# Optimization experiments

Measured on AMD Instinct MI355X. Metric: run time of the kernel, lower is better.

The kernel has to match this reference:

```python
import jax, jax.numpy as jnp
import numpy as np
from jax import lax

LAMBDA = 1.0
N_ITER = 100
N, PDIM, QDIM = 4096, 128, 128


def setup_inputs() -> dict:
    key = jax.random.key(0)
    k1, k2, k3, k4, k5, k6 = jax.random.split(key, 6)
    return {
        "U": jax.random.normal(k1, (N, PDIM), dtype=jnp.float32),
        "V": jax.random.normal(k2, (N, QDIM), dtype=jnp.float32),
        "W": jax.random.uniform(k3, (N, N), dtype=jnp.float32),
        "mu": jax.random.uniform(k4, (N, 1), dtype=jnp.float32),
        "nu": jax.random.uniform(k5, (N, 1), dtype=jnp.float32),
        "A": jax.random.normal(k6, (PDIM, QDIM), dtype=jnp.float32),
    }


def reference(U, V, W, mu, nu, A):
    # Cost matrix: C = softplus(W - U A V^T)  -> (n, n)
    UV = jnp.einsum('np,pq,mq->nm', U, A, V)
    C = jax.nn.softplus(W - UV)
    K = jnp.exp(-LAMBDA * C)

    def step(carry, _):
        a, b = carry
        a = mu / (K @ b)          # (n,1)
        b = nu / (K.T @ a)        # (n,1)
        return (a, b), None

    init = (jnp.ones_like(mu), jnp.ones_like(nu))
    (a, b), _ = lax.scan(step, init, None, length=N_ITER)

    # plan = diag(a) @ K @ diag(b)  ==  a * K * b^T (outer-product scaling)
    plan = a * K * b.T
    return plan
```

## Files before the change

kernel.cpp:

```cpp
#include <hip/hip_runtime.h>
#include <hip/hip_bf16.h>
#include <stdint.h>

#define NDIM 4096
#define PD   128
#define TS   64
#define LDP  (PD + 4)

__device__ __forceinline__ float bf2f(unsigned int u16) {
    union { unsigned int i; float f; } v; v.i = u16 << 16; return v.f;
}
__device__ __forceinline__ unsigned short f2bf(float f) {
    union { float f; unsigned int i; } v; v.f = f;
    unsigned int x = v.i;
    return (unsigned short)((x + 0x7fffu + ((x >> 16) & 1u)) >> 16);
}

__global__ __launch_bounds__(128) void ua_kernel(
    const float* __restrict__ U, const float* __restrict__ A, float* __restrict__ UA)
{
    __shared__ float us[PD];
    const int i = blockIdx.x;
    const int q = threadIdx.x;
    us[q] = U[i * PD + q];
    __syncthreads();
    float acc = 0.f;
    #pragma unroll 8
    for (int p = 0; p < PD; ++p) acc += us[p] * A[p * PD + q];
    UA[i * PD + q] = acc;
}

__global__ __launch_bounds__(256) void buildK_kernel(
    const float* __restrict__ UA, const float* __restrict__ V,
    const float* __restrict__ W, unsigned short* __restrict__ K,
    unsigned short* __restrict__ KT)
{
    __shared__ float UAs[TS][LDP];
    __shared__ float Vs[TS][LDP];
    __shared__ float tileT[TS][TS + 1];
    const int i0 = blockIdx.y * TS, j0 = blockIdx.x * TS;
    const int t = threadIdx.x;

    for (int idx = t; idx < TS * PD / 4; idx += 256) {
        const int r = idx >> 5;
        const int c = (idx & 31) << 2;
        *(float4*)&UAs[r][c] = *(const float4*)&UA[(size_t)(i0 + r) * PD + c];
        *(float4*)&Vs[r][c]  = *(const float4*)&V[(size_t)(j0 + r) * PD + c];
    }
    __syncthreads();

    const int tx = t & 15, ty = t >> 4;
    float acc[4][4] = {};
    for (int p = 0; p < PD; p += 4) {
        float4 a4[4], b4[4];
        #pragma unroll
        for (int ii = 0; ii < 4; ++ii) a4[ii] = *(const float4*)&UAs[ty + 16 * ii][p];
        #pragma unroll
        for (int jj = 0; jj < 4; ++jj) b4[jj] = *(const float4*)&Vs[tx + 16 * jj][p];
        #pragma unroll
        for (int ii = 0; ii < 4; ++ii)
            #pragma unroll
            for (int jj = 0; jj < 4; ++jj)
                acc[ii][jj] += a4[ii].x * b4[jj].x + a4[ii].y * b4[jj].y
                             + a4[ii].z * b4[jj].z + a4[ii].w * b4[jj].w;
    }

    #pragma unroll
    for (int ii = 0; ii < 4; ++ii) {
        const int i = ty + 16 * ii;
        #pragma unroll
        for (int jj = 0; jj < 4; ++jj) {
            const int j = tx + 16 * jj;
            const float w = W[(size_t)(i0 + i) * NDIM + (j0 + j)];
            const float k = 1.0f / (1.0f + __expf(w - acc[ii][jj]));
            K[(size_t)(i0 + i) * NDIM + (j0 + j)] = f2bf(k);
            tileT[j][i] = k;
        }
    }
    __syncthreads();
    for (int idx = t; idx < TS * TS; idx += 256) {
        const int j = idx >> 6, i = idx & 63;
        KT[(size_t)(j0 + j) * NDIM + (i0 + i)] = f2bf(tileT[j][i]);
    }
}

__global__ __launch_bounds__(256) void init_ones_kernel(float* __restrict__ v) {
    v[blockIdx.x * 256 + threadIdx.x] = 1.0f;
}

__global__ __launch_bounds__(256) void matvec_div_kernel(
    const unsigned short* __restrict__ M, const float* __restrict__ vin,
    const float* __restrict__ num, float* __restrict__ vout)
{
    const int wave = threadIdx.x >> 6;
    const int lane = threadIdx.x & 63;
    const int row  = blockIdx.x * 4 + wave;
    const unsigned short* mrow = M + (size_t)row * NDIM;
    float acc = 0.f;
    #pragma unroll
    for (int pass = 0; pass < NDIM / (64 * 8); ++pass) {
        const int j0 = (pass * 64 + lane) * 8;
        const uint4  kv = *(const uint4*)&mrow[j0];
        const float4 b0 = *(const float4*)&vin[j0];
        const float4 b1 = *(const float4*)&vin[j0 + 4];
        acc += bf2f(kv.x & 0xffffu) * b0.x;
        acc += bf2f(kv.x >> 16)     * b0.y;
        acc += bf2f(kv.y & 0xffffu) * b0.z;
        acc += bf2f(kv.y >> 16)     * b0.w;
        acc += bf2f(kv.z & 0xffffu) * b1.x;
        acc += bf2f(kv.z >> 16)     * b1.y;
        acc += bf2f(kv.w & 0xffffu) * b1.z;
        acc += bf2f(kv.w >> 16)     * b1.w;
    }
    #pragma unroll
    for (int off = 32; off > 0; off >>= 1) acc += __shfl_down(acc, off, 64);
    if (lane == 0) vout[row] = num[row] / acc;
}

__global__ __launch_bounds__(256) void plan_kernel(
    const float* __restrict__ UA, const float* __restrict__ V,
    const float* __restrict__ W, const float* __restrict__ av,
    const float* __restrict__ bv, float* __restrict__ out)
{
    __shared__ float UAs[TS][LDP];
    __shared__ float Vs[TS][LDP];
    const int i0 = blockIdx.y * TS, j0 = blockIdx.x * TS;
    const int t = threadIdx.x;

    for (int idx = t; idx < TS * PD / 4; idx += 256) {
        const int r = idx >> 5;
        const int c = (idx & 31) << 2;
        *(float4*)&UAs[r][c] = *(const float4*)&UA[(size_t)(i0 + r) * PD + c];
        *(float4*)&Vs[r][c]  = *(const float4*)&V[(size_t)(j0 + r) * PD + c];
    }
    __syncthreads();

    const int tx = t & 15, ty = t >> 4;
    float acc[4][4] = {};
    for (int p = 0; p < PD; p += 4) {
        float4 a4[4], b4[4];
        #pragma unroll
        for (int ii = 0; ii < 4; ++ii) a4[ii] = *(const float4*)&UAs[ty + 16 * ii][p];
        #pragma unroll
        for (int jj = 0; jj < 4; ++jj) b4[jj] = *(const float4*)&Vs[tx + 16 * jj][p];
        #pragma unroll
        for (int ii = 0; ii < 4; ++ii)
            #pragma unroll
            for (int jj = 0; jj < 4; ++jj)
                acc[ii][jj] += a4[ii].x * b4[jj].x + a4[ii].y * b4[jj].y
                             + a4[ii].z * b4[jj].z + a4[ii].w * b4[jj].w;
    }

    #pragma unroll
    for (int ii = 0; ii < 4; ++ii) {
        const int i = ty + 16 * ii;
        const float ai = av[i0 + i];
        #pragma unroll
        for (int jj = 0; jj < 4; ++jj) {
            const int j = tx + 16 * jj;
            const float w = W[(size_t)(i0 + i) * NDIM + (j0 + j)];
            const float k = 1.0f / (1.0f + expf(w - acc[ii][jj]));
            out[(size_t)(i0 + i) * NDIM + (j0 + j)] = ai * k * bv[j0 + j];
        }
    }
}

extern "C" void kernel_launch(void* const* d_in, const int* in_sizes, int n_in,
                              void* d_out, int out_size, void* d_ws, size_t ws_size,
                              hipStream_t stream) {
    const float* U  = (const float*)d_in[0];
    const float* V  = (const float*)d_in[1];
    const float* W  = (const float*)d_in[2];
    const float* mu = (const float*)d_in[3];
    const float* nu = (const float*)d_in[4];
    const float* A  = (const float*)d_in[5];
    float* out = (float*)d_out;

    unsigned short* K  = (unsigned short*)d_out;
    unsigned short* KT = K + (size_t)NDIM * NDIM;

    char* ws  = (char*)d_ws;
    float* UA = (float*)ws;
    float* av = (float*)(ws + (size_t)(2u << 20));
    float* bv = av + NDIM;

    ua_kernel<<<NDIM, PD, 0, stream>>>(U, A, UA);
    dim3 gridK(NDIM / TS, NDIM / TS);
    buildK_kernel<<<gridK, 256, 0, stream>>>(UA, V, W, K, KT);
    init_ones_kernel<<<NDIM / 256, 256, 0, stream>>>(bv);

    for (int it = 0; it < 100; ++it) {
        matvec_div_kernel<<<NDIM / 4, 256, 0, stream>>>(K,  bv, mu, av);
        matvec_div_kernel<<<NDIM / 4, 256, 0, stream>>>(KT, av, nu, bv);
    }

    plan_kernel<<<gridK, 256, 0, stream>>>(UA, V, W, av, bv, out);
}
```

Baseline: 1.736 ms.

## Quantize Sinkhorn kernel matrix to uint8 and cache fp32 K for the final plan

Stores K and its transpose as 8-bit linear-quantized values (k*255) instead of bf16, so each of the 200 matvecs reads half as many bytes. The 255 scale is folded back in the division. When the workspace is large enough, buildK also writes an fp32 copy of K, and an elementwise kernel forms the plan from it instead of recomputing the GEMM and softplus. The fp32 copy costs an extra 64MB write and read. The smem staging is also split into K-chunks, which reduces shared memory. Uniform 8-bit quantization loses relative precision for small K entries, so accuracy may suffer.

```diff
diff --git a/kernel.cpp b/kernel.cpp
--- a/kernel.cpp
+++ b/kernel.cpp
@@ -5,15 +5,67 @@
 #define NDIM 4096
 #define PD   128
 #define TS   64
-#define LDP  (PD + 4)
-
-__device__ __forceinline__ float bf2f(unsigned int u16) {
-    union { unsigned int i; float f; } v; v.i = u16 << 16; return v.f;
-}
-__device__ __forceinline__ unsigned short f2bf(float f) {
-    union { float f; unsigned int i; } v; v.f = f;
-    unsigned int x = v.i;
-    return (unsigned short)((x + 0x7fffu + ((x >> 16) & 1u)) >> 16);
+#define KC   64
+#define LDK  (KC + 4)
+
+__global__ __launch_bounds__(256) void buildK_kernel(
+    const float* __restrict__ UA, const float* __restrict__ V,
+    const float* __restrict__ W, unsigned char* __restrict__ K8,
+    unsigned char* __restrict__ KT8, float* __restrict__ K32)
+{
+    __shared__ float UAs[TS][LDK];
+    __shared__ float Vs[TS][LDK];
+    __shared__ float tileT[TS][TS + 1];
+    const int i0 = blockIdx.y * TS, j0 = blockIdx.x * TS;
+    const int t = threadIdx.x;
+    const int tx = t & 15, ty = t >> 4;
+
+    float acc[4][4] = {};
+    for (int kc = 0; kc < PD; kc += KC) {
+        for (int idx = t; idx < TS * (KC / 4); idx += 256) {
+            const int r = idx >> 4;
+            const int c = (idx & 15) << 2;
+            *(float4*)&UAs[r][c] = *(const float4*)&UA[(size_t)(i0 + r) * PD + kc + c];
+            *(float4*)&Vs[r][c]  = *(const float4*)&V[(size_t)(j0 + r) * PD + kc + c];
+        }
+        __syncthreads();
+        for (int p = 0; p < KC; p += 4) {
+            float4 a4[4], b4[4];
+            #pragma unroll
+            for (int ii = 0; ii < 4; ++ii) a4[ii] = *(const float4*)&UAs[ty + 16 * ii][p];
+            #pragma unroll
+            for (int jj = 0; jj < 4; ++jj) b4[jj] = *(const float4*)&Vs[tx + 16 * jj][p];
+            #pragma unroll
+            for (int ii = 0; ii < 4; ++ii)
+                #pragma unroll
+                for (int jj = 0; jj < 4; ++jj)
+                    acc[ii][jj] += a4[ii].x * b4[jj].x + a4[ii].y * b4[jj].y
+                                 + a4[ii].z * b4[jj].z + a4[ii].w * b4[jj].w;
+        }
+        __syncthreads();
+    }
+
+    #pragma unroll
+    for (int ii = 0; ii < 4; ++ii) {
+        const int i = ty + 16 * ii;
+        #pragma unroll
+        for (int jj = 0; jj < 4; ++jj) {
+            const int j = tx + 16 * jj;
+            const float w = W[(size_t)(i0 + i) * NDIM + (j0 + j)];
+            tileT[j][i] = 1.0f / (1.0f + __expf(w - acc[ii][jj]));
+        }
+    }
+    __syncthreads();
+    for (int idx = t; idx < TS * TS; idx += 256) {
+        const int j = idx >> 6, i = idx & 63;
+        KT8[(size_t)(j0 + j) * NDIM + (i0 + i)] = (unsigned char)(tileT[j][i] * 255.f + 0.5f);
+    }
+    for (int idx = t; idx < TS * TS; idx += 256) {
+        const int i = idx >> 6, j = idx & 63;
+        const float k = tileT[j][i];
+        K8[(size_t)(i0 + i) * NDIM + (j0 + j)] = (unsigned char)(k * 255.f + 0.5f);
+        if (K32) K32[(size_t)(i0 + i) * NDIM + (j0 + j)] = k;
+    }
 }
 
 __global__ __launch_bounds__(128) void ua_kernel(
@@ -30,137 +82,113 @@
     UA[i * PD + q] = acc;
 }
 
-__global__ __launch_bounds__(256) void buildK_kernel(
-    const float* __restrict__ UA, const float* __restrict__ V,
-    const float* __restrict__ W, unsigned short* __restrict__ K,
-    unsigned short* __restrict__ KT)
-{
-    __shared__ float UAs[TS][LDP];
-    __shared__ float Vs[TS][LDP];
-    __shared__ float tileT[TS][TS + 1];
-    const int i0 = blockIdx.y * TS, j0 = blockIdx.x * TS;
-    const int t = threadIdx.x;
-
-    for (int idx = t; idx < TS * PD / 4; idx += 256) {
-        const int r = idx >> 5;
-        const int c = (idx & 31) << 2;
-        *(float4*)&UAs[r][c] = *(const float4*)&UA[(size_t)(i0 + r) * PD + c];
-        *(float4*)&Vs[r][c]  = *(const float4*)&V[(size_t)(j0 + r) * PD + c];
-    }
-    __syncthreads();
-
-    const int tx = t & 15, ty = t >> 4;
-    float acc[4][4] = {};
-    for (int p = 0; p < PD; p += 4) {
-        float4 a4[4], b4[4];
-        #pragma unroll
-        for (int ii = 0; ii < 4; ++ii) a4[ii] = *(const float4*)&UAs[ty + 16 * ii][p];
-        #pragma unroll
-        for (int jj = 0; jj < 4; ++jj) b4[jj] = *(const float4*)&Vs[tx + 16 * jj][p];
-        #pragma unroll
-        for (int ii = 0; ii < 4; ++ii)
-            #pragma unroll
-            for (int jj = 0; jj < 4; ++jj)
-                acc[ii][jj] += a4[ii].x * b4[jj].x + a4[ii].y * b4[jj].y
-                             + a4[ii].z * b4[jj].z + a4[ii].w * b4[jj].w;
-    }
-
-    #pragma unroll
-    for (int ii = 0; ii < 4; ++ii) {
-        const int i = ty + 16 * ii;
-        #pragma unroll
-        for (int jj = 0; jj < 4; ++jj) {
-            const int j = tx + 16 * jj;
-            const float w = W[(size_t)(i0 + i) * NDIM + (j0 + j)];
-            const float k = 1.0f / (1.0f + __expf(w - acc[ii][jj]));
-            K[(size_t)(i0 + i) * NDIM + (j0 + j)] = f2bf(k);
-            tileT[j][i] = k;
-        }
-    }
-    __syncthreads();
-    for (int idx = t; idx < TS * TS; idx += 256) {
-        const int j = idx >> 6, i = idx & 63;
-        KT[(size_t)(j0 + j) * NDIM + (i0 + i)] = f2bf(tileT[j][i]);
-    }
-}
-
 __global__ __launch_bounds__(256) void init_ones_kernel(float* __restrict__ v) {
     v[blockIdx.x * 256 + threadIdx.x] = 1.0f;
 }
 
-__global__ __launch_bounds__(256) void matvec_div_kernel(
-    const unsigned short* __restrict__ M, const float* __restrict__ vin,
+__global__ __launch_bounds__(256) void matvec_u8_div_kernel(
+    const unsigned char* __restrict__ M, const float* __restrict__ vin,
     const float* __restrict__ num, float* __restrict__ vout)
 {
     const int wave = threadIdx.x >> 6;
     const int lane = threadIdx.x & 63;
     const int row  = blockIdx.x * 4 + wave;
-    const unsigned short* mrow = M + (size_t)row * NDIM;
+    const unsigned char* mrow = M + (size_t)row * NDIM;
     float acc = 0.f;
     #pragma unroll
-    for (int pass = 0; pass < NDIM / (64 * 8); ++pass) {
-        const int j0 = (pass * 64 + lane) * 8;
+    for (int pass = 0; pass < NDIM / (64 * 16); ++pass) {
+        const int j0 = (pass * 64 + lane) * 16;
         const uint4  kv = *(const uint4*)&mrow[j0];
         const float4 b0 = *(const float4*)&vin[j0];
         const float4 b1 = *(const float4*)&vin[j0 + 4];
-        acc += bf2f(kv.x & 0xffffu) * b0.x;
-        acc += bf2f(kv.x >> 16)     * b0.y;
-        acc += bf2f(kv.y & 0xffffu) * b0.z;
-        acc += bf2f(kv.y >> 16)     * b0.w;
-        acc += bf2f(kv.z & 0xffffu) * b1.x;
-        acc += bf2f(kv.z >> 16)     * b1.y;
-        acc += bf2f(kv.w & 0xffffu) * b1.z;
-        acc += bf2f(kv.w >> 16)     * b1.w;
+        const float4 b2 = *(const float4*)&vin[j0 + 8];
+        const float4 b3 = *(const float4*)&vin[j0 + 12];
+        acc += (float)( kv.x        & 0xffu) * b0.x;
+        acc += (float)((kv.x >>  8) & 0xffu) * b0.y;
+        acc += (float)((kv.x >> 16) & 0xffu) * b0.z;
+        acc += (float)( kv.x >> 24         ) * b0.w;
+        acc += (float)( kv.y        & 0xffu) * b1.x;
+        acc += (float)((kv.y >>  8) & 0xffu) * b1.y;
+        acc += (float)((kv.y >> 16) & 0xffu) * b1.z;
+        acc += (float)( kv.y >> 24         ) * b1.w;
+        acc += (float)( kv.z        & 0xffu) * b2.x;
+        acc += (float)((kv.z >>  8) & 0xffu) * b2.y;
+        acc += (float)((kv.z >> 16) & 0xffu) * b2.z;
+        acc += (float)( kv.z >> 24         ) * b2.w;
+        acc += (float)( kv.w        & 0xffu) * b3.x;
+        acc += (float)((kv.w >>  8) & 0xffu) * b3.y;
+        acc += (float)((kv.w >> 16) & 0xffu) * b3.z;
+        acc += (float)( kv.w >> 24         ) * b3.w;
     }
     #pragma unroll
     for (int off = 32; off > 0; off >>= 1) acc += __shfl_down(acc, off, 64);
-    if (lane == 0) vout[row] = num[row] / acc;
-}
-
-__global__ __launch_bounds__(256) void plan_kernel(
+    if (lane == 0) vout[row] = 255.0f * num[row] / acc;
+}
+
+__global__ __launch_bounds__(256) void plan_ew_kernel(
+    const float* __restrict__ K32, const float* __restrict__ av,
+    const float* __restrict__ bv, float* __restrict__ out)
+{
+    const size_t base = ((size_t)blockIdx.x * 256 + threadIdx.x) * 4;
+    const int i = (int)(base >> 12);
+    const int j = (int)(base & 4095);
+    const float a = av[i];
+    const float4 k4 = *(const float4*)&K32[base];
+    const float4 b4 = *(const float4*)&bv[j];
+    float4 o;
+    o.x = a * k4.x * b4.x;
+    o.y = a * k4.y * b4.y;
+    o.z = a * k4.z * b4.z;
+    o.w = a * k4.w * b4.w;
+    *(float4*)&out[base] = o;
+}
+
+__global__ __launch_bounds__(256) void plan_fb_kernel(
     const float* __restrict__ UA, const float* __restrict__ V,
     const float* __restrict__ W, const float* __restrict__ av,
     const float* __restrict__ bv, float* __restrict__ out)
 {
-    __shared__ float UAs[TS][LDP];
-    __shared__ float Vs[TS][LDP];
+    __shared__ float UAs[TS][LDK];
+    __shared__ float Vs[TS][LDK];
     const int i0 = blockIdx.y * TS, j0 = blockIdx.x * TS;
     const int t = threadIdx.x;
-
-    for (int idx = t; idx < TS * PD / 4; idx += 256) {
-        const int r = idx >> 5;
-        const int c = (idx & 31) << 2;
-        *(float4*)&UAs[r][c] = *(const float4*)&UA[(size_t)(i0 + r) * PD + c];
-        *(float4*)&Vs[r][c]  = *(const float4*)&V[(size_t)(j0 + r) * PD + c];
-    }
-    __syncthreads();
-
     const int tx = t & 15, ty = t >> 4;
+
     float acc[4][4] = {};
-    for (int p = 0; p < PD; p += 4) {
-        float4 a4[4], b4[4];
-        #pragma unroll
-        for (int ii = 0; ii < 4; ++ii) a4[ii] = *(const float4*)&UAs[ty + 16 * ii][p];
-        #pragma unroll
-        for (int jj = 0; jj < 4; ++jj) b4[jj] = *(const float4*)&Vs[tx + 16 * jj][p];
-        #pragma unroll
-        for (int ii = 0; ii < 4; ++ii)
-            #pragma unroll
-            for (int jj = 0; jj < 4; ++jj)
-                acc[ii][jj] += a4[ii].x * b4[jj].x + a4[ii].y * b4[jj].y
-                             + a4[ii].z * b4[jj].z + a4[ii].w * b4[jj].w;
+    for (int kc = 0; kc < PD; kc += KC) {
+        for (int idx = t; idx < TS * (KC / 4); idx += 256) {
+            const int r = idx >> 4;
+            const int c = (idx & 15) << 2;
+            *(float4*)&UAs[r][c] = *(const float4*)&UA[(size_t)(i0 + r) * PD + kc + c];
+            *(float4*)&Vs[r][c]  = *(const float4*)&V[(size_t)(j0 + r) * PD + kc + c];
+        }
+        __syncthreads();
+        for (int p = 0; p < KC; p += 4) {
+            float4 a4[4], b4[4];
+            #pragma unroll
+            for (int ii = 0; ii < 4; ++ii) a4[ii] = *(const float4*)&UAs[ty + 16 * ii][p];
+            #pragma unroll
+            for (int jj = 0; jj < 4; ++jj) b4[jj] = *(const float4*)&Vs[tx + 16 * jj][p];
+            #pragma unroll
+            for (int ii = 0; ii < 4; ++ii)
+                #pragma unroll
+                for (int jj = 0; jj < 4; ++jj)
+                    acc[ii][jj] += a4[ii].x * b4[jj].x + a4[ii].y * b4[jj].y
+                                 + a4[ii].z * b4[jj].z + a4[ii].w * b4[jj].w;
+        }
+        __syncthreads();
     }
 
     #pragma unroll
     for (int ii = 0; ii < 4; ++ii) {
         const int i = ty + 16 * ii;
-        const float ai = av[i0 + i];
+        const float a = av[i0 + i];
         #pragma unroll
         for (int jj = 0; jj < 4; ++jj) {
             const int j = tx + 16 * jj;
             const float w = W[(size_t)(i0 + i) * NDIM + (j0 + j)];
             const float k = 1.0f / (1.0f + expf(w - acc[ii][jj]));
-            out[(size_t)(i0 + i) * NDIM + (j0 + j)] = ai * k * bv[j0 + j];
+            out[(size_t)(i0 + i) * NDIM + (j0 + j)] = a * k * bv[j0 + j];
         }
     }
 }
@@ -176,23 +204,30 @@
     const float* A  = (const float*)d_in[5];
     float* out = (float*)d_out;
 
-    unsigned short* K  = (unsigned short*)d_out;
-    unsigned short* KT = K + (size_t)NDIM * NDIM;
-
-    char* ws  = (char*)d_ws;
-    float* UA = (float*)ws;
-    float* av = (float*)(ws + (size_t)(2u << 20));
-    float* bv = av + NDIM;
+    unsigned char* K8  = (unsigned char*)d_out;
+    unsigned char* KT8 = K8 + (size_t)NDIM * NDIM;
+
+    const size_t k32_bytes = (size_t)NDIM * NDIM * 4;
+    const size_t ua_bytes  = (size_t)NDIM * PD * 4;
+    const bool big = ws_size >= k32_bytes + ua_bytes + 3 * NDIM * 4;
+
+    char* ws   = (char*)d_ws;
+    float* K32 = big ? (float*)ws : nullptr;
+    char*  p   = ws + (big ? k32_bytes : 0);
+    float* UA  = (float*)p;
+    float* av  = (float*)(p + ua_bytes);
+    float* bv  = av + NDIM;
 
     ua_kernel<<<NDIM, PD, 0, stream>>>(U, A, UA);
     dim3 gridK(NDIM / TS, NDIM / TS);
-    buildK_kernel<<<gridK, 256, 0, stream>>>(UA, V, W, K, KT);
+    buildK_kernel<<<gridK, 256, 0, stream>>>(UA, V, W, K8, KT8, K32);
     init_ones_kernel<<<NDIM / 256, 256, 0, stream>>>(bv);
 
     for (int it = 0; it < 100; ++it) {
-        matvec_div_kernel<<<NDIM / 4, 256, 0, stream>>>(K,  bv, mu, av);
-        matvec_div_kernel<<<NDIM / 4, 256, 0, stream>>>(KT, av, nu, bv);
-    }
-
-    plan_kernel<<<gridK, 256, 0, stream>>>(UA, V, W, av, bv, out);
-}
+        matvec_u8_div_kernel<<<NDIM / 4, 256, 0, stream>>>(K8,  bv, mu, av);
+        matvec_u8_div_kernel<<<NDIM / 4, 256, 0, stream>>>(KT8, av, nu, bv);
+    }
+
+    if (big) plan_ew_kernel<<<(NDIM / 4) * (NDIM / 256), 256, 0, stream>>>(K32, av, bv, out);
+    else     plan_fb_kernel<<<gridK, 256, 0, stream>>>(UA, V, W, av, bv, out);
+}
```

After: 1.512 ms. -12.9%, faster.
